# Kernel optimization log

Measured on AMD Instinct MI355X. Metric: run time of the kernel, lower is better.

The kernel has to match this reference:

```python
import jax, jax.numpy as jnp
import numpy as np

IN_CHANNELS = 128
N_NODES = 100000
N_EDGES = 625000


def setup_inputs() -> dict:
    key = jax.random.key(0)
    k1, k2, k3, k4, k5, k6 = jax.random.split(key, 6)
    d = IN_CHANNELS
    x = jax.random.normal(k1, (N_NODES, d), dtype=jnp.float32)
    edge_index = jax.random.randint(k2, (2, N_EDGES), 0, N_NODES, dtype=jnp.int64)
    # Linear params, torch default init: U(-1/sqrt(fan_in), 1/sqrt(fan_in))
    b1_bound = 1.0 / np.sqrt(2 * d)
    W1 = jax.random.uniform(k3, (d, 2 * d), minval=-b1_bound, maxval=b1_bound, dtype=jnp.float32)
    b1 = jax.random.uniform(k4, (d,), minval=-b1_bound, maxval=b1_bound, dtype=jnp.float32)
    b2_bound = 1.0 / np.sqrt(d)
    W2 = jax.random.uniform(k5, (1, d), minval=-b2_bound, maxval=b2_bound, dtype=jnp.float32)
    b2 = jax.random.uniform(k6, (1,), minval=-b2_bound, maxval=b2_bound, dtype=jnp.float32)
    return {"x": x, "edge_index": edge_index, "W1": W1, "b1": b1, "W2": W2, "b2": b2}


def reference(x, edge_index, W1, b1, W2, b2):
    # Gather endpoint features and concat along feature dim: [E, 2d]
    h = jnp.concatenate([x[edge_index[0]], x[edge_index[1]]], axis=1)
    h = jax.nn.relu(h @ W1.T + b1)          # [E, d]
    h = jax.nn.relu(h @ W2.T + b2)          # [E, 1]
    return jax.nn.sigmoid(h)
```

## Files before the change

### kernel.cpp

```cpp
#include <hip/hip_runtime.h>
#include <hip/hip_bf16.h>
#include <hip/hip_fp16.h>
#include <math.h>


typedef short    s16x4 __attribute__((ext_vector_type(4)));
typedef short    s16x8 __attribute__((ext_vector_type(8)));
typedef float    f32x4 __attribute__((ext_vector_type(4)));
typedef _Float16 h16x2 __attribute__((ext_vector_type(2)));
typedef _Float16 h16x8 __attribute__((ext_vector_type(8)));

#define D    128
#define ALD  136
#define CWLD 80

static __device__ inline short f2bf(float f) {
    unsigned u = __builtin_bit_cast(unsigned, f);
    unsigned r = (u + 0x7FFFu + ((u >> 16) & 1u)) >> 16;
    return (short)r;
}

static __device__ inline unsigned enc1_sw(float f) {
    f = fminf(fmaxf(f, -448.f), 448.f);
    unsigned short h = __builtin_bit_cast(unsigned short, (_Float16)(f * (1.0f / 256.0f)));
    unsigned s = (h >> 8) & 0x80u;
    unsigned mag = h & 0x7FFFu;
    mag = mag + 0x3Fu + ((mag >> 7) & 1u);
    return s | ((mag >> 7) & 0x7Fu);
}
static __device__ inline unsigned enc2(float a, float b) {
#if __has_builtin(__builtin_amdgcn_cvt_pk_fp8_f32)
    return ((unsigned)__builtin_amdgcn_cvt_pk_fp8_f32(a, b, 0, false)) & 0xFFFFu;
#else
    return enc1_sw(a) | (enc1_sw(b) << 8);
#endif
}

#if __has_builtin(__builtin_amdgcn_cvt_pk_f16_fp8)
#define YSC 1.0f
static __device__ inline h16x2 dec2lo(unsigned v) {
    return __builtin_amdgcn_cvt_pk_f16_fp8((short)v);
}
static __device__ inline h16x2 dec2hi(unsigned v) {
    return __builtin_amdgcn_cvt_pk_f16_fp8((short)(v >> 16));
}
#else
#define YSC 256.0f
static __device__ inline h16x2 dec2lo(unsigned v) {
    unsigned p = __builtin_amdgcn_perm(0u, v, 0x0C010C00u);
    unsigned h = ((p << 8) & 0x80008000u) | ((p << 7) & 0x3F803F80u);
    return __builtin_bit_cast(h16x2, h);
}
static __device__ inline h16x2 dec2hi(unsigned v) {
    unsigned p = __builtin_amdgcn_perm(0u, v, 0x0C030C02u);
    unsigned h = ((p << 8) & 0x80008000u) | ((p << 7) & 0x3F803F80u);
    return __builtin_bit_cast(h16x2, h);
}
#endif

static __device__ inline h16x2 reluh(h16x2 v) {
#if __has_builtin(__builtin_elementwise_max)
    h16x2 z = { (_Float16)0.0f, (_Float16)0.0f };
    return __builtin_elementwise_max(v, z);
#else
    unsigned u = __builtin_bit_cast(unsigned, v);
    unsigned m = ((u >> 15) & 0x00010001u) * 0xFFFFu;
    u &= ~m;
    return __builtin_bit_cast(h16x2, u);
#endif
}

static __device__ inline float dot2acc(h16x2 a, h16x2 b, float c) {
#if __has_builtin(__builtin_amdgcn_fdot2)
    return __builtin_amdgcn_fdot2(a, b, c, false);
#else
    return c + (float)a[0] * (float)b[0] + (float)a[1] * (float)b[1];
#endif
}

__global__ __launch_bounds__(256) void pack_w1_kernel(
    const float* __restrict__ W1, short* __restrict__ W1F)
{
    int g    = blockIdx.x * 256 + threadIdx.x;
    int lane = g & 63;
    int c    = (g >> 6) & 3;
    int j    = (g >> 8) & 3;
    int cs   = g >> 10;
    int o    = cs * 64 + j * 16 + (lane & 15);
    int kb   = c * 32 + (lane >> 4) * 8;
    const float* wp = W1 + (size_t)(o & 127) * 256 + (o >> 7) * 128 + kb;
    float4 u0 = *(const float4*)wp;
    float4 u1 = *(const float4*)(wp + 4);
    s16x8 v = { f2bf(u0.x), f2bf(u0.y), f2bf(u0.z), f2bf(u0.w),
                f2bf(u1.x), f2bf(u1.y), f2bf(u1.z), f2bf(u1.w) };
    *(s16x8*)&W1F[(size_t)g * 8] = v;
}

__global__ __launch_bounds__(256) void precompute_kernel(
    const float* __restrict__ x,
    const short* __restrict__ W1F,
    const float* __restrict__ b1,
    unsigned char* __restrict__ Y8,
    int N, int ntiles)
{
    __shared__ short    At[32 * ALD];
    __shared__ _Float16 Cw[4][32 * CWLD];

    const int tid  = threadIdx.x;
    const int wid  = tid >> 6;
    const int lane = tid & 63;
    const int quad = lane >> 4, l15 = lane & 15;
    const int cs   = wid;

    s16x8 bf[4][4];
    #pragma unroll
    for (int j = 0; j < 4; ++j)
        #pragma unroll
        for (int c = 0; c < 4; ++c)
            bf[c][j] = *(const s16x8*)&W1F[(size_t)(((cs * 4 + j) * 4 + c) * 64 + lane) * 8];
    float b1v[4];
    #pragma unroll
    for (int j = 0; j < 4; ++j)
        b1v[j] = (cs < 2) ? b1[cs * 64 + j * 16 + l15] : 0.f;

    const int srow = tid >> 3;
    const int sc0  = (tid & 7) * 4;
    _Float16* cw = &Cw[wid][0];

    int t = blockIdx.x;
    float4 xv[4];
    if (t < ntiles) {
        int m = t * 32 + srow; if (m >= N) m = N - 1;
        const float* xp = &x[(size_t)m * D + sc0];
        #pragma unroll
        for (int p = 0; p < 4; ++p)
            xv[p] = *(const float4*)(xp + p * 32);
    }

    while (t < ntiles) {
        const int m0 = t * 32;
        const int tn = t + gridDim.x;

        #pragma unroll
        for (int p = 0; p < 4; ++p) {
            s16x4 bv = { f2bf(xv[p].x), f2bf(xv[p].y), f2bf(xv[p].z), f2bf(xv[p].w) };
            *(s16x4*)&At[srow * ALD + sc0 + p * 32] = bv;
        }
        __syncthreads();

        if (tn < ntiles) {
            int m = tn * 32 + srow; if (m >= N) m = N - 1;
            const float* xp = &x[(size_t)m * D + sc0];
            #pragma unroll
            for (int p = 0; p < 4; ++p)
                xv[p] = *(const float4*)(xp + p * 32);
        }

        f32x4 acc[2][4] = {};
        #pragma unroll
        for (int c = 0; c < 4; ++c) {
            const int kc = c * 32;
            s16x8 af[2];
            #pragma unroll
            for (int i = 0; i < 2; ++i)
                af[i] = *(const s16x8*)&At[(i * 16 + l15) * ALD + kc + quad * 8];
            #pragma unroll
            for (int i = 0; i < 2; ++i)
                #pragma unroll
                for (int j = 0; j < 4; ++j)
                    acc[i][j] = __builtin_amdgcn_mfma_f32_16x16x32_bf16(
                        af[i], bf[c][j], acc[i][j], 0, 0, 0);
        }

        #pragma unroll
        for (int i = 0; i < 2; ++i)
            #pragma unroll
            for (int j = 0; j < 4; ++j)
                #pragma unroll
                for (int r = 0; r < 4; ++r)
                    cw[(i * 16 + quad * 4 + r) * CWLD + j * 16 + l15] =
                        (_Float16)(acc[i][j][r] + b1v[j]);

        #pragma unroll
        for (int p = 0; p < 2; ++p) {
            int row = p * 16 + (lane >> 2);
            int m   = m0 + row;
            if (m < N) {
                const _Float16* sp = &cw[row * CWLD + (lane & 3) * 16];
                uint4 ov;
                unsigned dw[4];
                #pragma unroll
                for (int q = 0; q < 4; ++q)
                    dw[q] = enc2((float)sp[q*4+0], (float)sp[q*4+1])
                          | (enc2((float)sp[q*4+2], (float)sp[q*4+3]) << 16);
                ov.x = dw[0]; ov.y = dw[1]; ov.z = dw[2]; ov.w = dw[3];
                *(uint4*)&Y8[(size_t)m * 256 + cs * 64 + (lane & 3) * 16] = ov;
            }
        }

        __syncthreads();
        t = tn;
    }
}

#define EPB 128

__global__ __launch_bounds__(256) void edge_kernel(
    const unsigned char* __restrict__ Y8,
    const int*           __restrict__ ei,
    const float*         __restrict__ W2,
    const float*         __restrict__ b2,
    float*               __restrict__ out,
    int E)
{
    const int tid = threadIdx.x;
    const int sub = tid & 7;
    const int grp = tid >> 3;
    const int e0  = blockIdx.x * EPB + grp;

    h16x2 w2h[8];
    {
        const float* wp = &W2[sub * 16];
        #pragma unroll
        for (int q = 0; q < 8; ++q) {
            float2 f = *(const float2*)(wp + q * 2);
            w2h[q] = (h16x2){ (_Float16)(f.x * YSC), (_Float16)(f.y * YSC) };
        }
    }

    int  ee[4]; bool vv[4]; uint4 L[4], R[4];
    #pragma unroll
    for (int k = 0; k < 4; ++k) {
        ee[k] = e0 + 32 * k;
        vv[k] = (ee[k] < E);
        int src = vv[k] ? ei[ee[k]] : 0;
        int dst = vv[k] ? ei[E + ee[k]] : 0;
        L[k] = *(const uint4*)(Y8 + (size_t)src * 256 + sub * 16);
        R[k] = *(const uint4*)(Y8 + (size_t)dst * 256 + 128 + sub * 16);
    }

    float s[4] = { 0.f, 0.f, 0.f, 0.f };
    #pragma unroll
    for (int k = 0; k < 4; ++k) {
        const unsigned* a = (const unsigned*)&L[k];
        const unsigned* c = (const unsigned*)&R[k];
        #pragma unroll
        for (int d = 0; d < 4; ++d) {
            h16x2 za = reluh(dec2lo(a[d]) + dec2lo(c[d]));
            s[k] = dot2acc(za, w2h[2*d],     s[k]);
            h16x2 zb = reluh(dec2hi(a[d]) + dec2hi(c[d]));
            s[k] = dot2acc(zb, w2h[2*d + 1], s[k]);
        }
    }

    #pragma unroll
    for (int k = 0; k < 4; ++k) {
        s[k] += __shfl_xor(s[k], 1);
        s[k] += __shfl_xor(s[k], 2);
        s[k] += __shfl_xor(s[k], 4);
    }

    if (sub == 0) {
        float bb = b2[0];
        #pragma unroll
        for (int k = 0; k < 4; ++k) {
            if (vv[k]) {
                float t = fmaxf(s[k] + bb, 0.f);
                out[ee[k]] = 1.0f / (1.0f + expf(-t));
            }
        }
    }
}

#define BM   128
#define BK   64
#define LDT  72

__global__ __launch_bounds__(256) void decoder_fallback_kernel(
    const float* __restrict__ x, const int* __restrict__ ei,
    const float* __restrict__ W1, const float* __restrict__ b1,
    const float* __restrict__ W2, const float* __restrict__ b2,
    float* __restrict__ out, int E)
{
    __shared__ int   nid[2][BM];
    __shared__ short At[BM * LDT];
    __shared__ short Bt[D * LDT];
    __shared__ float rowsum[BM][2];

    const int tid = threadIdx.x;
    const int e0  = blockIdx.x * BM;
    if (tid < BM) { int e = e0 + tid; nid[0][tid] = (e < E) ? ei[e] : 0; }
    else { int e = e0 + (tid - BM); nid[1][tid - BM] = (e < E) ? ei[E + e] : 0; }

    const int wid = tid >> 6, lane = tid & 63;
    const int wm = wid >> 1, wn = wid & 1;
    const int quad = lane >> 4, l15 = lane & 15;
    const int srow = tid >> 4, scol = (tid & 15) * 4;
    f32x4 acc[4][4] = {};
    __syncthreads();

    for (int t = 0; t < 4; ++t) {
        const int* ids = nid[t >> 1];
        const int kx = (t & 1) * BK, kw = t * BK;
        #pragma unroll
        for (int p = 0; p < 8; ++p) {
            int row = srow + p * 16;
            float4 v = *(const float4*)&x[(size_t)ids[row] * D + kx + scol];
            s16x4 bv = { f2bf(v.x), f2bf(v.y), f2bf(v.z), f2bf(v.w) };
            *(s16x4*)&At[row * LDT + scol] = bv;
        }
        #pragma unroll
        for (int p = 0; p < 8; ++p) {
            int n = srow + p * 16;
            float4 v = *(const float4*)&W1[n * 256 + kw + scol];
            s16x4 bv = { f2bf(v.x), f2bf(v.y), f2bf(v.z), f2bf(v.w) };
            *(s16x4*)&Bt[n * LDT + scol] = bv;
        }
        __syncthreads();
        #pragma unroll
        for (int c = 0; c < 2; ++c) {
            const int kc = c * 32;
            s16x8 af[4], bfr[4];
            #pragma unroll
            for (int i = 0; i < 4; ++i)
                af[i] = *(const s16x8*)&At[(wm*64 + i*16 + l15) * LDT + kc + quad*8];
            #pragma unroll
            for (int j = 0; j < 4; ++j)
                bfr[j] = *(const s16x8*)&Bt[(wn*64 + j*16 + l15) * LDT + kc + quad*8];
            #pragma unroll
            for (int i = 0; i < 4; ++i)
                #pragma unroll
                for (int j = 0; j < 4; ++j)
                    acc[i][j] = __builtin_amdgcn_mfma_f32_16x16x32_bf16(
                        af[i], bfr[j], acc[i][j], 0, 0, 0);
        }
        __syncthreads();
    }
    float b1v[4], w2v[4];
    #pragma unroll
    for (int j = 0; j < 4; ++j) {
        int col = wn*64 + j*16 + l15;
        b1v[j] = b1[col]; w2v[j] = W2[col];
    }
    float psum[16];
    #pragma unroll
    for (int t = 0; t < 16; ++t) psum[t] = 0.f;
    #pragma unroll
    for (int i = 0; i < 4; ++i)
        #pragma unroll
        for (int j = 0; j < 4; ++j)
            #pragma unroll
            for (int r = 0; r < 4; ++r) {
                float c = fmaxf(acc[i][j][r] + b1v[j], 0.f);
                psum[i*4 + r] += c * w2v[j];
            }
    #pragma unroll
    for (int off = 1; off < 16; off <<= 1)
        #pragma unroll
        for (int t = 0; t < 16; ++t)
            psum[t] += __shfl_xor(psum[t], off);
    if (l15 == 0) {
        #pragma unroll
        for (int i = 0; i < 4; ++i)
            #pragma unroll
            for (int r = 0; r < 4; ++r)
                rowsum[wm*64 + i*16 + quad*4 + r][wn] = psum[i*4 + r];
    }
    __syncthreads();
    if (tid < BM) {
        int e = e0 + tid;
        if (e < E) {
            float s = rowsum[tid][0] + rowsum[tid][1] + b2[0];
            s = fmaxf(s, 0.f);
            out[e] = 1.0f / (1.0f + expf(-s));
        }
    }
}

extern "C" void kernel_launch(void* const* d_in, const int* in_sizes, int n_in,
                              void* d_out, int out_size, void* d_ws, size_t ws_size,
                              hipStream_t stream) {
    const float* x  = (const float*)d_in[0];
    const int*   ei = (const int*)d_in[1];
    const float* W1 = (const float*)d_in[2];
    const float* b1 = (const float*)d_in[3];
    const float* W2 = (const float*)d_in[4];
    const float* b2 = (const float*)d_in[5];
    float* out = (float*)d_out;

    int E = in_sizes[1] / 2;
    int N = in_sizes[0] / D;

    size_t y_bytes = (size_t)N * 256;
    size_t need    = y_bytes + 32768 * sizeof(short);
    if (ws_size >= need) {
        unsigned char* Y8  = (unsigned char*)d_ws;
        short*         W1F = (short*)((char*)d_ws + y_bytes);
        pack_w1_kernel<<<16, 256, 0, stream>>>(W1, W1F);
        int ntiles = (N + 31) / 32;
        int gridA  = (ntiles + 3) / 4;
        precompute_kernel<<<gridA, 256, 0, stream>>>(x, W1F, b1, Y8, N, ntiles);
        int gridB = (E + EPB - 1) / EPB;
        edge_kernel<<<gridB, 256, 0, stream>>>(Y8, ei, W2, b2, out, E);
    } else {
        int nblocks = (E + BM - 1) / BM;
        decoder_fallback_kernel<<<nblocks, 256, 0, stream>>>(
            x, ei, W1, b1, W2, b2, out, E);
    }
}
```

Baseline: 134.3 us.

## Double-buffer precompute A tile and write FP8 output directly from transposed MFMA

The precompute kernel now uses two LDS buffers for the bf16 x tile. The next tile is converted and stored while the current one is consumed, which removes one __syncthreads per iteration. The MFMA operands are swapped so each lane holds four consecutive output columns, and the fp16 LDS staging buffer for the epilogue is dropped. Bias plus FP8 packing is written straight to global memory as 4-byte stores, in exchange for narrower, less coalesced stores than the previous 16-byte writes.

New measurement: 140.5 us. 1.05x slower.

```diff
diff --git a/kernel.cpp b/kernel.cpp
--- a/kernel.cpp
+++ b/kernel.cpp
@@ -8,11 +8,9 @@
 typedef short    s16x8 __attribute__((ext_vector_type(8)));
 typedef float    f32x4 __attribute__((ext_vector_type(4)));
 typedef _Float16 h16x2 __attribute__((ext_vector_type(2)));
-typedef _Float16 h16x8 __attribute__((ext_vector_type(8)));
 
 #define D    128
 #define ALD  136
-#define CWLD 80
 
 static __device__ inline short f2bf(float f) {
     unsigned u = __builtin_bit_cast(unsigned, f);
@@ -103,8 +101,7 @@
     unsigned char* __restrict__ Y8,
     int N, int ntiles)
 {
-    __shared__ short    At[32 * ALD];
-    __shared__ _Float16 Cw[4][32 * CWLD];
+    __shared__ short At[2][32 * ALD];
 
     const int tid  = threadIdx.x;
     const int wid  = tid >> 6;
@@ -118,35 +115,37 @@
         #pragma unroll
         for (int c = 0; c < 4; ++c)
             bf[c][j] = *(const s16x8*)&W1F[(size_t)(((cs * 4 + j) * 4 + c) * 64 + lane) * 8];
-    float b1v[4];
-    #pragma unroll
-    for (int j = 0; j < 4; ++j)
-        b1v[j] = (cs < 2) ? b1[cs * 64 + j * 16 + l15] : 0.f;
+
+    f32x4 b1v[4];
+    #pragma unroll
+    for (int j = 0; j < 4; ++j) {
+        if (cs < 2) b1v[j] = *(const f32x4*)&b1[cs * 64 + j * 16 + quad * 4];
+        else        b1v[j] = (f32x4){0.f, 0.f, 0.f, 0.f};
+    }
 
     const int srow = tid >> 3;
     const int sc0  = (tid & 7) * 4;
-    _Float16* cw = &Cw[wid][0];
+    const int g    = gridDim.x;
 
     int t = blockIdx.x;
     float4 xv[4];
-    if (t < ntiles) {
+    {
         int m = t * 32 + srow; if (m >= N) m = N - 1;
         const float* xp = &x[(size_t)m * D + sc0];
         #pragma unroll
         for (int p = 0; p < 4; ++p)
             xv[p] = *(const float4*)(xp + p * 32);
     }
-
+    #pragma unroll
+    for (int p = 0; p < 4; ++p) {
+        s16x4 bv = { f2bf(xv[p].x), f2bf(xv[p].y), f2bf(xv[p].z), f2bf(xv[p].w) };
+        *(s16x4*)&At[0][srow * ALD + sc0 + p * 32] = bv;
+    }
+    __syncthreads();
+
+    int buf = 0;
     while (t < ntiles) {
-        const int m0 = t * 32;
-        const int tn = t + gridDim.x;
-
-        #pragma unroll
-        for (int p = 0; p < 4; ++p) {
-            s16x4 bv = { f2bf(xv[p].x), f2bf(xv[p].y), f2bf(xv[p].z), f2bf(xv[p].w) };
-            *(s16x4*)&At[srow * ALD + sc0 + p * 32] = bv;
-        }
-        __syncthreads();
+        const int tn = t + g;
 
         if (tn < ntiles) {
             int m = tn * 32 + srow; if (m >= N) m = N - 1;
@@ -159,46 +158,42 @@
         f32x4 acc[2][4] = {};
         #pragma unroll
         for (int c = 0; c < 4; ++c) {
-            const int kc = c * 32;
             s16x8 af[2];
             #pragma unroll
             for (int i = 0; i < 2; ++i)
-                af[i] = *(const s16x8*)&At[(i * 16 + l15) * ALD + kc + quad * 8];
+                af[i] = *(const s16x8*)&At[buf][(i * 16 + l15) * ALD + c * 32 + quad * 8];
             #pragma unroll
             for (int i = 0; i < 2; ++i)
                 #pragma unroll
                 for (int j = 0; j < 4; ++j)
                     acc[i][j] = __builtin_amdgcn_mfma_f32_16x16x32_bf16(
-                        af[i], bf[c][j], acc[i][j], 0, 0, 0);
-        }
-
-        #pragma unroll
-        for (int i = 0; i < 2; ++i)
-            #pragma unroll
-            for (int j = 0; j < 4; ++j)
+                        bf[c][j], af[i], acc[i][j], 0, 0, 0);
+        }
+
+        const int m0 = t * 32;
+        #pragma unroll
+        for (int i = 0; i < 2; ++i) {
+            int m = m0 + i * 16 + l15;
+            if (m < N) {
+                unsigned char* yp = Y8 + (size_t)m * 256 + cs * 64 + quad * 4;
                 #pragma unroll
-                for (int r = 0; r < 4; ++r)
-                    cw[(i * 16 + quad * 4 + r) * CWLD + j * 16 + l15] =
-                        (_Float16)(acc[i][j][r] + b1v[j]);
-
-        #pragma unroll
-        for (int p = 0; p < 2; ++p) {
-            int row = p * 16 + (lane >> 2);
-            int m   = m0 + row;
-            if (m < N) {
-                const _Float16* sp = &cw[row * CWLD + (lane & 3) * 16];
-                uint4 ov;
-                unsigned dw[4];
-                #pragma unroll
-                for (int q = 0; q < 4; ++q)
-                    dw[q] = enc2((float)sp[q*4+0], (float)sp[q*4+1])
-                          | (enc2((float)sp[q*4+2], (float)sp[q*4+3]) << 16);
-                ov.x = dw[0]; ov.y = dw[1]; ov.z = dw[2]; ov.w = dw[3];
-                *(uint4*)&Y8[(size_t)m * 256 + cs * 64 + (lane & 3) * 16] = ov;
+                for (int j = 0; j < 4; ++j) {
+                    f32x4 v = acc[i][j] + b1v[j];
+                    unsigned dw = enc2(v[0], v[1]) | (enc2(v[2], v[3]) << 16);
+                    *(unsigned*)(yp + j * 16) = dw;
+                }
             }
         }
 
+        if (tn < ntiles) {
+            #pragma unroll
+            for (int p = 0; p < 4; ++p) {
+                s16x4 bv = { f2bf(xv[p].x), f2bf(xv[p].y), f2bf(xv[p].z), f2bf(xv[p].w) };
+                *(s16x4*)&At[buf ^ 1][srow * ALD + sc0 + p * 32] = bv;
+            }
+        }
         __syncthreads();
+        buf ^= 1;
         t = tn;
     }
 }
```
